# Optimization experiments

Hardware: AMD Instinct MI355X
Metric: run time of the kernel (lower is better)

Reference implementation:

```python
import jax, jax.numpy as jnp
from jax import lax
import numpy as np

L, P = 156, 8
NUM_EMB, EMB_DIM = 512, 8
COMMIT = 0.25
B, H, W = 16, 128, 128


def conv2d(x, w, b):
    # x: NCHW, w: OIHW, 3x3, stride 1, pad 1 (same)
    y = lax.conv_general_dilated(x, w, (1, 1), ((1, 1), (1, 1)),
                                 dimension_numbers=('NCHW', 'OIHW', 'NCHW'))
    return y + b[None, :, None, None]


def convT2d(x, w, b):
    # torch ConvTranspose2d weight: (in, out, kH, kW), k=3, s=1, p=1.
    # Equivalent to a regular SAME conv with spatially-flipped, IO-swapped kernel.
    w_eff = jnp.transpose(jnp.flip(w, (2, 3)), (1, 0, 2, 3))  # OIHW
    return conv2d(x, w_eff, b)


def setup_inputs() -> dict:
    key = jax.random.key(0)
    ks = jax.random.split(key, 14)
    x = jax.random.uniform(ks[0], (B, L, H, W), dtype=jnp.float32)

    def wconv(k, o, i):
        return jax.random.normal(k, (o, i, 3, 3), dtype=jnp.float32) * 0.05

    inp = {
        'x': x,
        # encoder (Conv2d, OIHW)
        'e1_w': wconv(ks[1], P * 16, L), 'e1_b': jnp.zeros((P * 16,), jnp.float32),
        'e2_w': wconv(ks[2], P * 8, P * 16), 'e2_b': jnp.zeros((P * 8,), jnp.float32),
        'e3_w': wconv(ks[3], P, P * 8), 'e3_b': jnp.zeros((P,), jnp.float32),
        # codebook, torch init uniform(-1/K, 1/K)
        'emb': jax.random.uniform(ks[4], (NUM_EMB, EMB_DIM), jnp.float32,
                                  -1.0 / NUM_EMB, 1.0 / NUM_EMB),
        # decoder (ConvTranspose2d, weight shape (in, out, kH, kW))
        'd1_w': jax.random.normal(ks[5], (P, P * 8, 3, 3), jnp.float32) * 0.05,
        'd1_b': jnp.zeros((P * 8,), jnp.float32),
        'd2_w': jax.random.normal(ks[6], (P * 8, P * 16, 3, 3), jnp.float32) * 0.05,
        'd2_b': jnp.zeros((P * 16,), jnp.float32),
        'd3_w': jax.random.normal(ks[7], (P * 16, L, 3, 3), jnp.float32) * 0.05,
        'd3_b': jnp.zeros((L,), jnp.float32),
    }
    return inp


def reference(x, e1_w, e1_b, e2_w, e2_b, e3_w, e3_b, emb,
              d1_w, d1_b, d2_w, d2_b, d3_w, d3_b):
    # encoder
    z = jax.nn.relu(conv2d(x, e1_w, e1_b))
    z = jax.nn.relu(conv2d(z, e2_w, e2_b))
    z = jax.nn.relu(conv2d(z, e3_w, e3_b))

    # vector quantizer (flatten NCHW order, exactly like torch .view)
    flat = z.reshape(-1, EMB_DIM)  # [N, D]
    dists = (jnp.sum(flat * flat, axis=1, keepdims=True)
             + jnp.sum(emb * emb, axis=1)
             - 2.0 * flat @ emb.T)  # [N, K]
    idx = jnp.argmin(dists, axis=1)  # [N]
    quantized = emb[idx].reshape(z.shape)

    e_latent_loss = jnp.mean((lax.stop_gradient(quantized) - z) ** 2)
    q_latent_loss = jnp.mean((quantized - lax.stop_gradient(z)) ** 2)
    vq_loss = q_latent_loss + COMMIT * e_latent_loss

    # decoder
    y = jax.nn.relu(convT2d(quantized, d1_w, d1_b))
    y = jax.nn.relu(convT2d(y, d2_w, d2_b))
    x_hat = jax.nn.sigmoid(convT2d(y, d3_w, d3_b))
    return x_hat, vq_loss
```

## Files before the change

### kernel.cpp

```cpp
#include <hip/hip_runtime.h>
#include <hip/hip_bf16.h>


typedef __bf16 bf16x8 __attribute__((ext_vector_type(8)));
typedef float  floatx4 __attribute__((ext_vector_type(4)));

__device__ __forceinline__ unsigned short f2bf(float f) {
    return __builtin_bit_cast(unsigned short, __float2bfloat16(f));
}
__device__ __forceinline__ float bf2f(unsigned short u) {
    return __bfloat162float(__builtin_bit_cast(__hip_bfloat16, u));
}

__device__ __forceinline__ void gload_lds16(const void* g, void* l) {
    __builtin_amdgcn_global_load_lds(
        (const __attribute__((address_space(1))) void*)g,
        (__attribute__((address_space(3))) void*)l, 16, 0, 0);
}

__global__ __launch_bounds__(256) void xpose_k(const float* __restrict__ x,
                                               unsigned short* __restrict__ xn)
{
    __shared__ unsigned short t[64 * 168];
    const int b = blockIdx.y;
    const int hw0 = blockIdx.x * 64;
    const int cl = threadIdx.x >> 6;
    const int hwl = threadIdx.x & 63;
    #pragma unroll 4
    for (int cc = 0; cc < 40; ++cc) {
        int c = cc * 4 + cl;
        float v = (c < 156) ? x[((size_t)(b * 156 + c) << 14) + hw0 + hwl] : 0.0f;
        t[hwl * 168 + c] = f2bf(v);
    }
    __syncthreads();
    for (int i = threadIdx.x; i < 64 * 20; i += 256) {
        int row = i / 20, qq = i - row * 20;
        uint4 v = *(const uint4*)(t + row * 168 + qq * 8);
        *(uint4*)(xn + ((size_t)((b << 14) + hw0 + row)) * 160 + qq * 8) = v;
    }
}

__global__ __launch_bounds__(256) void repack_k(const float* __restrict__ w,
                                                unsigned short* __restrict__ wr,
                                                int Cout, int Cin, int OCP, int ICP,
                                                int trans, int n)
{
    int i = blockIdx.x * 256 + threadIdx.x;
    if (i >= n) return;
    int ic = i % ICP, rest = i / ICP;
    int oc = rest % OCP, tap = rest / OCP;
    float v = 0.0f;
    if (oc < Cout && ic < Cin) {
        v = trans ? w[(size_t)(ic * Cout + oc) * 9 + (8 - tap)]
                  : w[(size_t)(oc * Cin + ic) * 9 + tap];
    }
    wr[i] = f2bf(v);
}

__global__ void zero_k(float* p) { *p = 0.0f; }
__global__ __launch_bounds__(256) void zero4_k(uint4* __restrict__ p, int n4)
{
    int i = blockIdx.x * 256 + threadIdx.x;
    if (i < n4) p[i] = uint4{0, 0, 0, 0};
}

template <int ICP, int OCB, int OMODE, int OUTC>
__global__ __launch_bounds__(256, 2) void conv_mfma(const unsigned short* __restrict__ in,
                                                    const unsigned short* __restrict__ wrep,
                                                    const float* __restrict__ bias,
                                                    void* __restrict__ outv, int OCP,
                                                    const unsigned short* __restrict__ zpad)
{
    constexpr int NOT = OCB / 16;
    constexpr int NPH = ICP / 32;
    constexpr int NB  = (NPH > 1) ? 2 : 1;
    constexpr int WCH = 9 * OCB * 4;
    __shared__ unsigned short tile[NB][1296 * 8];
    __shared__ unsigned short wlds[WCH * 8];

    const int tid  = threadIdx.x;
    const int lane = tid & 63, wave = tid >> 6;
    const int col  = lane & 15, quad = lane >> 4;
    const int qsh  = quad << 4;
    const int ocblk = blockIdx.x, tix = blockIdx.y, b = blockIdx.z;
    const int h0 = (tix >> 3) << 4, w0 = (tix & 7) << 4;

    floatx4 acc[NOT][4];
    #pragma unroll
    for (int i = 0; i < NOT; ++i)
        #pragma unroll
        for (int r = 0; r < 4; ++r) acc[i][r] = floatx4{0.f, 0.f, 0.f, 0.f};

    int goff[5];
    #pragma unroll
    for (int s = 0; s < 5; ++s) {
        int c = tid + (s << 8);
        int p = c >> 2, m = c & 3;
        int q = m ^ ((p >> 1) & 3);
        int pr = p / 18, pc = p - pr * 18;
        int gh = h0 - 1 + pr, gw = w0 - 1 + pc;
        bool ok = ((unsigned)gh < 128u) & ((unsigned)gw < 128u);
        goff[s] = ok ? ((((b << 7) + gh) << 7) + gw) * ICP + (q << 3) : -1;
    }

    auto stage_in = [&](int bufi, int icc) {
        unsigned short* base = &tile[bufi][wave * 512];
        #pragma unroll
        for (int s = 0; s < 5; ++s) {
            const unsigned short* src =
                (goff[s] >= 0) ? in + (size_t)goff[s] + icc * 32 : zpad;
            gload_lds16(src, base + s * 2048);
        }
        if (tid < 16) {
            int c = 1280 + tid;
            int p = c >> 2, m = c & 3;
            int q = m ^ ((p >> 1) & 3);
            int pc = p - 306;
            int gh = h0 + 16, gw = w0 - 1 + pc;
            uint4 v = uint4{0, 0, 0, 0};
            if ((unsigned)gh < 128u && (unsigned)gw < 128u)
                v = *(const uint4*)(in +
                    (size_t)((((b << 7) + gh) << 7) + gw) * ICP + icc * 32 + (q << 3));
            *(uint4*)(&tile[bufi][c << 3]) = v;
        }
    };

    auto stage_w = [&](int icc) {
        #pragma unroll
        for (int s = 0; s < (WCH + 255) / 256; ++s) {
            int c = tid + (s << 8);
            bool on = (WCH % 256 == 0) || (c < WCH);
            if (on) {
                int tap = c / (OCB * 4);
                int rest = c - tap * (OCB * 4);
                int oc = rest >> 2, m = rest & 3;
                int q = m ^ ((oc >> 1) & 3);
                const unsigned short* src = wrep +
                    ((size_t)(tap * OCP + ocblk * OCB + oc)) * ICP + icc * 32 + (q << 3);
                gload_lds16(src, &wlds[(size_t)((s << 8) + wave * 64) * 8]);
            }
        }
    };

    const int aswz = (col << 6) + ((quad ^ ((col >> 1) & 3)) << 4);

    auto compute_ph = [&](int bufi) {
        const unsigned short* tb = &tile[bufi][0];
        #pragma unroll
        for (int tap = 0; tap < 9; ++tap) {
            const int dh = tap / 3, dw = tap % 3;
            bf16x8 bfr[4];
            #pragma unroll
            for (int rt = 0; rt < 4; ++rt) {
                int p = ((wave << 2) + rt + dh) * 18 + col + dw;
                int boff = (p << 6) ^ qsh ^ ((p & 6) << 3);
                bfr[rt] = *(const bf16x8*)((const char*)tb + boff);
            }
            #pragma unroll
            for (int ot = 0; ot < NOT; ++ot) {
                bf16x8 afr = *(const bf16x8*)((const char*)wlds +
                    tap * (OCB * 64) + (ot << 10) + aswz);
                #pragma unroll
                for (int rt = 0; rt < 4; ++rt)
                    acc[ot][rt] = __builtin_amdgcn_mfma_f32_16x16x32_bf16(
                        afr, bfr[rt], acc[ot][rt], 0, 0, 0);
            }
        }
    };

    stage_in(0, 0);
    stage_w(0);
    asm volatile("s_waitcnt vmcnt(0)" ::: "memory");
    __syncthreads();
    #pragma unroll
    for (int icc = 0; icc < NPH; ++icc) {
        const int cur = icc & 1;
        if (icc + 1 < NPH) stage_in(cur ^ 1, icc + 1);
        compute_ph(cur);
        if (icc + 1 < NPH) {
            __syncthreads();
            stage_w(icc + 1);
            asm volatile("s_waitcnt vmcnt(0)" ::: "memory");
            __syncthreads();
        }
    }

    const int w = w0 + col;
    #pragma unroll
    for (int ot = 0; ot < NOT; ++ot) {
        int oc0 = ocblk * OCB + (ot << 4) + (quad << 2);
        #pragma unroll
        for (int rt = 0; rt < 4; ++rt) {
            int h = h0 + (wave << 2) + rt;
            if constexpr (OMODE == 0) {
                unsigned short* outp = (unsigned short*)outv;
                unsigned short pk[4];
                #pragma unroll
                for (int g = 0; g < 4; ++g) {
                    float vv = acc[ot][rt][g] + bias[oc0 + g];
                    pk[g] = f2bf(fmaxf(vv, 0.0f));
                }
                size_t off = ((size_t)(((b << 7) + h) << 7) + w) * OUTC + oc0;
                *(uint2*)(outp + off) = *(const uint2*)pk;
            } else if constexpr (OMODE == 1) {
                unsigned short* outp = (unsigned short*)outv;
                #pragma unroll
                for (int g = 0; g < 4; ++g) {
                    int oc = oc0 + g;
                    if (oc < OUTC) {
                        float vv = fmaxf(acc[ot][rt][g] + bias[oc], 0.0f);
                        outp[((size_t)(b * OUTC + oc) << 14) + (h << 7) + w] = f2bf(vv);
                    }
                }
            } else {
                float* outp = (float*)outv;
                #pragma unroll
                for (int g = 0; g < 4; ++g) {
                    int oc = oc0 + g;
                    if (oc < OUTC) {
                        float vv = acc[ot][rt][g] + bias[oc];
                        vv = 1.0f / (1.0f + __expf(-vv));
                        outp[((size_t)(b * OUTC + oc) << 14) + (h << 7) + w] = vv;
                    }
                }
            }
        }
    }
}

__global__ __launch_bounds__(256) void vq_k(const unsigned short* __restrict__ z,
                                            const float* __restrict__ emb,
                                            unsigned short* __restrict__ q,
                                            float* __restrict__ loss)
{
    __shared__ float se[512 * 8];
    __shared__ float se2[512];
    __shared__ float red[4];

    for (int i = threadIdx.x; i < 4096; i += 256) se[i] = emb[i];
    __syncthreads();
    for (int k = threadIdx.x; k < 512; k += 256) {
        float s = 0.0f;
        #pragma unroll
        for (int j = 0; j < 8; ++j) { float e = se[k * 8 + j]; s += e * e; }
        se2[k] = s;
    }
    __syncthreads();

    int r = blockIdx.x * 256 + threadIdx.x;
    uint4 raw = *(const uint4*)(z + (size_t)r * 8);
    const unsigned short* pr = (const unsigned short*)&raw;
    float zv[8];
    #pragma unroll
    for (int j = 0; j < 8; ++j) zv[j] = bf2f(pr[j]);

    float best = 3.4e38f;
    int bi = 0;
    for (int k = 0; k < 512; ++k) {
        float dot = 0.0f;
        #pragma unroll
        for (int j = 0; j < 8; ++j) dot += se[k * 8 + j] * zv[j];
        float d = se2[k] - 2.0f * dot;
        if (d < best) { best = d; bi = k; }
    }

    int wg = r & 15, h = (r >> 4) & 127, c = (r >> 11) & 7, b = r >> 14;
    size_t pixbase = ((size_t)(((b << 7) + h) << 7)) + (wg << 3);
    float lsum = 0.0f;
    #pragma unroll
    for (int j = 0; j < 8; ++j) {
        float e = se[bi * 8 + j];
        q[(pixbase + j) * 32 + c] = f2bf(e);
        float df = e - zv[j];
        lsum += df * df;
    }

    for (int o = 32; o > 0; o >>= 1) lsum += __shfl_down(lsum, o, 64);
    int lane = threadIdx.x & 63, wv = threadIdx.x >> 6;
    if (lane == 0) red[wv] = lsum;
    __syncthreads();
    if (threadIdx.x == 0) atomicAdd(loss, red[0] + red[1] + red[2] + red[3]);
}

__global__ void fin_k(const float* __restrict__ loss, float* __restrict__ out)
{
    out[0] = 1.25f * (*loss) / 2097152.0f;
}

extern "C" void kernel_launch(void* const* d_in, const int* in_sizes, int n_in,
                              void* d_out, int out_size, void* d_ws, size_t ws_size,
                              hipStream_t stream)
{
    const float* x   = (const float*)d_in[0];
    const float* e1w = (const float*)d_in[1];
    const float* e1b = (const float*)d_in[2];
    const float* e2w = (const float*)d_in[3];
    const float* e2b = (const float*)d_in[4];
    const float* e3w = (const float*)d_in[5];
    const float* e3b = (const float*)d_in[6];
    const float* emb = (const float*)d_in[7];
    const float* d1w = (const float*)d_in[8];
    const float* d1b = (const float*)d_in[9];
    const float* d2w = (const float*)d_in[10];
    const float* d2b = (const float*)d_in[11];
    const float* d3w = (const float*)d_in[12];
    const float* d3b = (const float*)d_in[13];
    float* out = (float*)d_out;

    char* ws = (char*)d_ws;
    size_t off = 0;
    auto alloc = [&](size_t bytes) { void* p = ws + off; off += (bytes + 255) & ~size_t(255); return p; };

    float*          loss  = (float*)alloc(4);
    unsigned short* zpad  = (unsigned short*)alloc(512);
    unsigned short* wr_e1 = (unsigned short*)alloc((size_t)9 * 128 * 160 * 2);
    unsigned short* wr_e2 = (unsigned short*)alloc((size_t)9 * 64 * 128 * 2);
    unsigned short* wr_e3 = (unsigned short*)alloc((size_t)9 * 16 * 64 * 2);
    unsigned short* wr_d1 = (unsigned short*)alloc((size_t)9 * 64 * 32 * 2);
    unsigned short* wr_d2 = (unsigned short*)alloc((size_t)9 * 128 * 64 * 2);
    unsigned short* wr_d3 = (unsigned short*)alloc((size_t)9 * 192 * 128 * 2);
    unsigned short* z3    = (unsigned short*)alloc((size_t)16 * 8 * 16384 * 2);
    unsigned short* qb    = (unsigned short*)alloc((size_t)16 * 16384 * 32 * 2);
    unsigned short* S1    = (unsigned short*)alloc((size_t)16 * 16384 * 160 * 2);
    unsigned short* S2    = (unsigned short*)alloc((size_t)16 * 16384 * 128 * 2);
    (void)ws_size;

    zero_k<<<1, 1, 0, stream>>>(loss);
    zero4_k<<<1, 256, 0, stream>>>((uint4*)zpad, 32);
    zero4_k<<<(16 * 16384 * 32 / 8 + 255) / 256, 256, 0, stream>>>((uint4*)qb, 16 * 16384 * 32 / 8);

    xpose_k<<<dim3(256, 16), 256, 0, stream>>>(x, S1);

    auto rp = [&](const float* w, unsigned short* wr, int Cout, int Cin, int OCP, int ICP, int trans) {
        int n = 9 * OCP * ICP;
        repack_k<<<(n + 255) / 256, 256, 0, stream>>>(w, wr, Cout, Cin, OCP, ICP, trans, n);
    };
    rp(e1w, wr_e1, 128, 156, 128, 160, 0);
    rp(e2w, wr_e2,  64, 128,  64, 128, 0);
    rp(e3w, wr_e3,   8,  64,  16,  64, 0);
    rp(d1w, wr_d1,  64,   8,  64,  32, 1);
    rp(d2w, wr_d2, 128,  64, 128,  64, 1);
    rp(d3w, wr_d3, 156, 128, 192, 128, 1);

    conv_mfma<160, 64, 0, 128><<<dim3(2, 64, 16), 256, 0, stream>>>(S1, wr_e1, e1b, S2, 128, zpad);
    conv_mfma<128, 64, 0,  64><<<dim3(1, 64, 16), 256, 0, stream>>>(S2, wr_e2, e2b, S1, 64, zpad);
    conv_mfma< 64, 16, 1,   8><<<dim3(1, 64, 16), 256, 0, stream>>>(S1, wr_e3, e3b, z3, 16, zpad);
    vq_k<<<1024, 256, 0, stream>>>(z3, emb, qb, loss);
    conv_mfma< 32, 64, 0,  64><<<dim3(1, 64, 16), 256, 0, stream>>>(qb, wr_d1, d1b, S1, 64, zpad);
    conv_mfma< 64, 64, 0, 128><<<dim3(2, 64, 16), 256, 0, stream>>>(S1, wr_d2, d2b, S2, 128, zpad);
    conv_mfma<128, 64, 2, 156><<<dim3(3, 64, 16), 256, 0, stream>>>(S2, wr_d3, d3b, out, 192, zpad);

    fin_k<<<1, 1, 0, stream>>>(loss, out + (size_t)16 * 156 * 16384);
}
```

Baseline: 760.9 us.

## Double spatial tile height to 32 rows and drop input double buffering

Each conv block now computes a 32x16 output tile, with 8 row-tiles per wave, instead of 16x16. This halves the halo overhead and doubles the reuse of each loaded weight fragment, and the grid shrinks to match. To fit the larger input tile (34x18 halo) in LDS, the double-buffered input staging is replaced by a single buffer with a load, wait, sync, compute sequence, so load/compute overlap inside a block is lost. Register pressure roughly doubles in accumulators, which may hurt occupancy under launch_bounds(256,2).

```diff
diff --git a/kernel.cpp b/kernel.cpp
--- a/kernel.cpp
+++ b/kernel.cpp
@@ -72,10 +72,10 @@
                                                     const unsigned short* __restrict__ zpad)
 {
     constexpr int NOT = OCB / 16;
+    constexpr int RT  = 8;
     constexpr int NPH = ICP / 32;
-    constexpr int NB  = (NPH > 1) ? 2 : 1;
     constexpr int WCH = 9 * OCB * 4;
-    __shared__ unsigned short tile[NB][1296 * 8];
+    __shared__ unsigned short tile[2448 * 8];
     __shared__ unsigned short wlds[WCH * 8];
 
     const int tid  = threadIdx.x;
@@ -83,17 +83,17 @@
     const int col  = lane & 15, quad = lane >> 4;
     const int qsh  = quad << 4;
     const int ocblk = blockIdx.x, tix = blockIdx.y, b = blockIdx.z;
-    const int h0 = (tix >> 3) << 4, w0 = (tix & 7) << 4;
-
-    floatx4 acc[NOT][4];
+    const int h0 = (tix >> 3) << 5, w0 = (tix & 7) << 4;
+
+    floatx4 acc[NOT][RT];
     #pragma unroll
     for (int i = 0; i < NOT; ++i)
         #pragma unroll
-        for (int r = 0; r < 4; ++r) acc[i][r] = floatx4{0.f, 0.f, 0.f, 0.f};
-
-    int goff[5];
-    #pragma unroll
-    for (int s = 0; s < 5; ++s) {
+        for (int r = 0; r < RT; ++r) acc[i][r] = floatx4{0.f, 0.f, 0.f, 0.f};
+
+    int goff[9];
+    #pragma unroll
+    for (int s = 0; s < 9; ++s) {
         int c = tid + (s << 8);
         int p = c >> 2, m = c & 3;
         int q = m ^ ((p >> 1) & 3);
@@ -103,25 +103,25 @@
         goff[s] = ok ? ((((b << 7) + gh) << 7) + gw) * ICP + (q << 3) : -1;
     }
 
-    auto stage_in = [&](int bufi, int icc) {
-        unsigned short* base = &tile[bufi][wave * 512];
-        #pragma unroll
-        for (int s = 0; s < 5; ++s) {
+    auto stage_in = [&](int icc) {
+        unsigned short* base = &tile[wave * 512];
+        #pragma unroll
+        for (int s = 0; s < 9; ++s) {
             const unsigned short* src =
                 (goff[s] >= 0) ? in + (size_t)goff[s] + icc * 32 : zpad;
             gload_lds16(src, base + s * 2048);
         }
-        if (tid < 16) {
-            int c = 1280 + tid;
+        if (tid < 144) {
+            int c = 2304 + tid;
             int p = c >> 2, m = c & 3;
             int q = m ^ ((p >> 1) & 3);
-            int pc = p - 306;
-            int gh = h0 + 16, gw = w0 - 1 + pc;
+            int pr = p / 18, pc = p - pr * 18;
+            int gh = h0 - 1 + pr, gw = w0 - 1 + pc;
             uint4 v = uint4{0, 0, 0, 0};
             if ((unsigned)gh < 128u && (unsigned)gw < 128u)
                 v = *(const uint4*)(in +
                     (size_t)((((b << 7) + gh) << 7) + gw) * ICP + icc * 32 + (q << 3));
-            *(uint4*)(&tile[bufi][c << 3]) = v;
+            *(uint4*)(&tile[c << 3]) = v;
         }
     };
 
@@ -144,45 +144,37 @@
 
     const int aswz = (col << 6) + ((quad ^ ((col >> 1) & 3)) << 4);
 
-    auto compute_ph = [&](int bufi) {
-        const unsigned short* tb = &tile[bufi][0];
+    auto compute_ph = [&]() {
         #pragma unroll
         for (int tap = 0; tap < 9; ++tap) {
             const int dh = tap / 3, dw = tap % 3;
-            bf16x8 bfr[4];
+            bf16x8 bfr[RT];
             #pragma unroll
-            for (int rt = 0; rt < 4; ++rt) {
-                int p = ((wave << 2) + rt + dh) * 18 + col + dw;
+            for (int rt = 0; rt < RT; ++rt) {
+                int p = ((wave << 3) + rt + dh) * 18 + col + dw;
                 int boff = (p << 6) ^ qsh ^ ((p & 6) << 3);
-                bfr[rt] = *(const bf16x8*)((const char*)tb + boff);
+                bfr[rt] = *(const bf16x8*)((const char*)tile + boff);
             }
             #pragma unroll
             for (int ot = 0; ot < NOT; ++ot) {
                 bf16x8 afr = *(const bf16x8*)((const char*)wlds +
                     tap * (OCB * 64) + (ot << 10) + aswz);
                 #pragma unroll
-                for (int rt = 0; rt < 4; ++rt)
+                for (int rt = 0; rt < RT; ++rt)
                     acc[ot][rt] = __builtin_amdgcn_mfma_f32_16x16x32_bf16(
                         afr, bfr[rt], acc[ot][rt], 0, 0, 0);
             }
         }
     };
 
-    stage_in(0, 0);
-    stage_w(0);
-    asm volatile("s_waitcnt vmcnt(0)" ::: "memory");
-    __syncthreads();
     #pragma unroll
     for (int icc = 0; icc < NPH; ++icc) {
-        const int cur = icc & 1;
-        if (icc + 1 < NPH) stage_in(cur ^ 1, icc + 1);
-        compute_ph(cur);
-        if (icc + 1 < NPH) {
-            __syncthreads();
-            stage_w(icc + 1);
-            asm volatile("s_waitcnt vmcnt(0)" ::: "memory");
-            __syncthreads();
-        }
+        if (icc) __syncthreads();
+        stage_in(icc);
+        stage_w(icc);
+        asm volatile("s_waitcnt vmcnt(0)" ::: "memory");
+        __syncthreads();
+        compute_ph();
     }
 
     const int w = w0 + col;
@@ -190,8 +182,8 @@
     for (int ot = 0; ot < NOT; ++ot) {
         int oc0 = ocblk * OCB + (ot << 4) + (quad << 2);
         #pragma unroll
-        for (int rt = 0; rt < 4; ++rt) {
-            int h = h0 + (wave << 2) + rt;
+        for (int rt = 0; rt < RT; ++rt) {
+            int h = h0 + (wave << 3) + rt;
             if constexpr (OMODE == 0) {
                 unsigned short* outp = (unsigned short*)outv;
                 unsigned short pk[4];
@@ -342,13 +334,13 @@
     rp(d2w, wr_d2, 128,  64, 128,  64, 1);
     rp(d3w, wr_d3, 156, 128, 192, 128, 1);
 
-    conv_mfma<160, 64, 0, 128><<<dim3(2, 64, 16), 256, 0, stream>>>(S1, wr_e1, e1b, S2, 128, zpad);
-    conv_mfma<128, 64, 0,  64><<<dim3(1, 64, 16), 256, 0, stream>>>(S2, wr_e2, e2b, S1, 64, zpad);
-    conv_mfma< 64, 16, 1,   8><<<dim3(1, 64, 16), 256, 0, stream>>>(S1, wr_e3, e3b, z3, 16, zpad);
+    conv_mfma<160, 64, 0, 128><<<dim3(2, 32, 16), 256, 0, stream>>>(S1, wr_e1, e1b, S2, 128, zpad);
+    conv_mfma<128, 64, 0,  64><<<dim3(1, 32, 16), 256, 0, stream>>>(S2, wr_e2, e2b, S1, 64, zpad);
+    conv_mfma< 64, 16, 1,   8><<<dim3(1, 32, 16), 256, 0, stream>>>(S1, wr_e3, e3b, z3, 16, zpad);
     vq_k<<<1024, 256, 0, stream>>>(z3, emb, qb, loss);
-    conv_mfma< 32, 64, 0,  64><<<dim3(1, 64, 16), 256, 0, stream>>>(qb, wr_d1, d1b, S1, 64, zpad);
-    conv_mfma< 64, 64, 0, 128><<<dim3(2, 64, 16), 256, 0, stream>>>(S1, wr_d2, d2b, S2, 128, zpad);
-    conv_mfma<128, 64, 2, 156><<<dim3(3, 64, 16), 256, 0, stream>>>(S2, wr_d3, d3b, out, 192, zpad);
+    conv_mfma< 32, 64, 0,  64><<<dim3(1, 32, 16), 256, 0, stream>>>(qb, wr_d1, d1b, S1, 64, zpad);
+    conv_mfma< 64, 64, 0, 128><<<dim3(2, 32, 16), 256, 0, stream>>>(S1, wr_d2, d2b, S2, 128, zpad);
+    conv_mfma<128, 64, 2, 156><<<dim3(3, 32, 16), 256, 0, stream>>>(S2, wr_d3, d3b, out, 192, zpad);
 
     fin_k<<<1, 1, 0, stream>>>(loss, out + (size_t)16 * 156 * 16384);
 }
```

After: 1.107 ms. 1.46x slower.
